# Optimization experiments

Hardware: AMD Instinct MI355X
Metric: run time of the kernel (lower is better)

The kernel has to match this reference:

```python
import jax, jax.numpy as jnp
import numpy as np

B, P, C, UP = 4, 512, 384, 4
K1, K2, KR = 16, 8, 16
NOISE_SCALE = 0.02


def setup_inputs() -> dict:
    key = jax.random.key(0)
    ks = jax.random.split(key, 32)
    w = lambda i, s: (jax.random.normal(ks[i], s, jnp.float32) * 0.02)
    return {
        "ctx_xyz": jax.random.normal(ks[0], (B, P, 3), jnp.float32),
        "ctx_tokens": jax.random.normal(ks[1], (B, P, C), jnp.float32),
        "pred_xyz": jax.random.normal(ks[2], (B, P, 3), jnp.float32),
        "pred_token": jax.random.normal(ks[3], (B, P, C), jnp.float32),
        "noise": jax.random.normal(ks[4], (B, P * UP, 3), jnp.float32),
        "conv1_w1": w(5, (2 * C, C // 2)), "conv1_b1": jnp.zeros((C // 2,), jnp.float32),
        "conv1_w2": w(6, (C // 2, C // 2)), "conv1_b2": jnp.zeros((C // 2,), jnp.float32),
        "conv2_w1": w(7, (2 * (C // 2), C // 4)), "conv2_b1": jnp.zeros((C // 4,), jnp.float32),
        "conv2_w2": w(8, (C // 4, C // 4)), "conv2_b2": jnp.zeros((C // 4,), jnp.float32),
        "cdef_w1": w(9, (C // 4, C // 4)), "cdef_b1": jnp.zeros((C // 4,), jnp.float32),
        "cdef_w2": w(10, (C // 4, 3)), "cdef_b2": jnp.zeros((3,), jnp.float32),
        "fold_w1": w(11, (C // 4 + 3, 256)), "fold_b1": jnp.zeros((256,), jnp.float32),
        "fold_w2": w(12, (256, 256)), "fold_b2": jnp.zeros((256,), jnp.float32),
        "fold_w3": w(13, (256, 3)), "fold_b3": jnp.zeros((3,), jnp.float32),
        "ref_w1": w(14, (2 * (C // 4 + 3), C)), "ref_b1": jnp.zeros((C,), jnp.float32),
        "ref_w2": w(15, (C, 3)), "ref_b2": jnp.zeros((3,), jnp.float32),
    }


def knn_idx(x, k):
    # x: [N, D]; k nearest neighbors by L2, no self-loops (as knn_graph loop=False)
    sq = jnp.sum(x * x, axis=1)
    d = sq[:, None] + sq[None, :] - 2.0 * (x @ x.T)  # [N, N]
    n = x.shape[0]
    d = d.at[jnp.arange(n), jnp.arange(n)].set(jnp.inf)
    return jax.lax.top_k(-d, k)[1]  # [N, k]


def edge_max(x, idx, mlp):
    # EdgeConv: out[i] = max_j mlp([x_i, x_j - x_i])
    n, k = idx.shape
    xi = jnp.broadcast_to(x[:, None, :], (n, k, x.shape[1]))
    xj = x[idx]  # [N, k, D]
    return jnp.max(mlp(jnp.concatenate([xi, xj - xi], axis=-1)), axis=1)


def mlp2(w1, b1, w2, b2):
    return lambda t: jnp.maximum(t @ w1 + b1, 0.0) @ w2 + b2


def reference(ctx_xyz, ctx_tokens, pred_xyz, pred_token, noise,
              conv1_w1, conv1_b1, conv1_w2, conv1_b2,
              conv2_w1, conv2_b1, conv2_w2, conv2_b2,
              cdef_w1, cdef_b1, cdef_w2, cdef_b2,
              fold_w1, fold_b1, fold_w2, fold_b2, fold_w3, fold_b3,
              ref_w1, ref_b1, ref_w2, ref_b2):
    def shared_edgeconv(x):
        h = edge_max(x, knn_idx(x, K1), mlp2(conv1_w1, conv1_b1, conv1_w2, conv1_b2))
        return edge_max(h, knn_idx(h, K2), mlp2(conv2_w1, conv2_b1, conv2_w2, conv2_b2))

    # context branch
    ctx_xyz_f = ctx_xyz.reshape(-1, 3)
    ctx_tok_f = ctx_tokens.reshape(-1, C)
    ctx_feat = shared_edgeconv(ctx_tok_f)                       # [B*P, C//4]
    ctx_xyz_out = ctx_xyz_f + 0.05 * mlp2(cdef_w1, cdef_b1, cdef_w2, cdef_b2)(ctx_feat)

    # target branch: upsample + assign tokens
    tgt_xyz = (jnp.repeat(pred_xyz, UP, axis=1) + NOISE_SCALE * noise).reshape(-1, 3)
    tgt_tok = jnp.repeat(ctx_tokens, UP, axis=1).reshape(-1, C)
    tgt_feat = shared_edgeconv(tgt_tok)                         # [B*P*UP, C//4]

    # folding MLP (Linear-ReLU-Linear-ReLU-Linear) residual
    h = jnp.concatenate([tgt_xyz, tgt_feat], axis=-1)
    h = jnp.maximum(h @ fold_w1 + fold_b1, 0.0)
    h = jnp.maximum(h @ fold_w2 + fold_b2, 0.0)
    tgt_xyz = tgt_xyz + h @ fold_w3 + fold_b3

    # GNN refiner: knn over xyz, EdgeConv over [feat, xyz]
    idx = knn_idx(tgt_xyz, KR)
    xcat = jnp.concatenate([tgt_feat, tgt_xyz], axis=-1)
    tgt_xyz = tgt_xyz + edge_max(xcat, idx, mlp2(ref_w1, ref_b1, ref_w2, ref_b2))

    return jnp.concatenate([ctx_xyz_out, tgt_xyz], axis=0)
```

## Files before the change

kernel.cpp:

```cpp
#include <hip/hip_runtime.h>

#define N2 2048
#define N8 8192
#define CDIM 384
#define H1C 192
#define H2C 96
#define PDIM 512
#define KRR 16
#define FOLDH 256
#define XCAP 256
#define XTILE 1024
#define INFF 3.0e38f

__device__ __forceinline__ float frelu(float x) { return x > 0.f ? x : 0.f; }

__device__ __forceinline__ void bitonic64_val(float& d, int lane) {
    #pragma unroll
    for (int k = 2; k <= 64; k <<= 1) {
        #pragma unroll
        for (int j = k >> 1; j > 0; j >>= 1) {
            float od = __shfl_xor(d, j);
            bool lower = (lane & j) == 0;
            bool olt = od < d;
            bool take = lower ? olt : !olt;
            if (lane & k) take = !take;
            if (take) d = od;
        }
    }
}

__device__ __forceinline__ void bitonic64_pair(float& d, int& c, int lane) {
    #pragma unroll
    for (int k = 2; k <= 64; k <<= 1) {
        #pragma unroll
        for (int j = k >> 1; j > 0; j >>= 1) {
            float od = __shfl_xor(d, j);
            int   oc = __shfl_xor(c, j);
            bool lower = (lane & j) == 0;
            bool olt = (od < d) || (od == d && oc < c);
            bool take = lower ? olt : !olt;
            if (lane & k) take = !take;
            if (take) { d = od; c = oc; }
        }
    }
}

__device__ __forceinline__ void select_slow(const float* bd, const int* bi, int cnt,
                                            int ksel, int row, int n, int* out, int lane) {
    float cd[4]; int cix[4];
    #pragma unroll
    for (int s = 0; s < 4; ++s) {
        int c = lane + 64*s;
        bool v = c < cnt;
        cd[s]  = v ? bd[c] : INFF;
        cix[s] = v ? bi[c] : 0x7fffffff;
    }
    for (int r = 0; r < ksel; ++r) {
        float lv = cd[0]; int li = cix[0];
        #pragma unroll
        for (int s = 1; s < 4; ++s) {
            if (cd[s] < lv || (cd[s] == lv && cix[s] < li)) { lv = cd[s]; li = cix[s]; }
        }
        float wv = lv; int wi = li;
        #pragma unroll
        for (int s = 1; s < 64; s <<= 1) {
            float ov = __shfl_xor(wv, s); int oi = __shfl_xor(wi, s);
            if (ov < wv || (ov == wv && oi < wi)) { wv = ov; wi = oi; }
        }
        if (lane == 0) {
            int safe = ((unsigned)wi < (unsigned)n) ? wi : ((row + 1) & (n - 1));
            out[row*ksel + r] = safe;
        }
        #pragma unroll
        for (int s = 0; s < 4; ++s) {
            if (cd[s] == wv && cix[s] == wi) { cd[s] = INFF; cix[s] = 0x7fffffff; }
        }
    }
}

__global__ __launch_bounds__(256) void rowsq_kernel(const float* __restrict__ x,
                                                    float* __restrict__ sq, int d) {
    int wave = threadIdx.x >> 6, lane = threadIdx.x & 63;
    int row = blockIdx.x*4 + wave;
    float acc = 0.f;
    for (int k = lane; k < d; k += 64) { float v = x[(size_t)row*d + k]; acc += v*v; }
    #pragma unroll
    for (int s = 1; s < 64; s <<= 1) acc += __shfl_xor(acc, s);
    if (lane == 0) sq[row] = acc;
}

__global__ __launch_bounds__(256) void rowsqpair_kernel(const float* __restrict__ xA,
                                                        float* __restrict__ sqA,
                                                        const float* __restrict__ xB,
                                                        float* __restrict__ sqB, int d) {
    const float* x = blockIdx.y ? xB : xA;
    float* sq = blockIdx.y ? sqB : sqA;
    int wave = threadIdx.x >> 6, lane = threadIdx.x & 63;
    int row = blockIdx.x*4 + wave;
    float acc = 0.f;
    for (int k = lane; k < d; k += 64) { float v = x[(size_t)row*d + k]; acc += v*v; }
    #pragma unroll
    for (int s = 1; s < 64; s <<= 1) acc += __shfl_xor(acc, s);
    if (lane == 0) sq[row] = acc;
}

__device__ __forceinline__ void disttri_body(const float* __restrict__ x, const float* __restrict__ sq,
                                             float* __restrict__ dist, int n, int K) {
    int l = blockIdx.x;
    int by = (int)((sqrtf(8.f*(float)l + 1.f) - 1.f)*0.5f);
    while ((by+1)*(by+2)/2 <= l) ++by;
    while (by*(by+1)/2 > l) --by;
    int bx = l - by*(by+1)/2;
    int row0 = by*64, col0 = bx*64;
    __shared__ __align__(16) float As[16][68];
    __shared__ __align__(16) float Bs[16][68];
    __shared__ __align__(16) float T[64][68];
    int tx = threadIdx.x, ty = threadIdx.y;
    int t = ty*16 + tx;
    float acc[4][4] = {};
    for (int k0 = 0; k0 < K; k0 += 16) {
        #pragma unroll
        for (int r = 0; r < 4; ++r) {
            int e = t + 256*r; int kk = e & 15, mm = e >> 4;
            As[kk][mm] = x[(size_t)(row0+mm)*K + k0+kk];
            Bs[kk][mm] = x[(size_t)(col0+mm)*K + k0+kk];
        }
        __syncthreads();
        #pragma unroll
        for (int kk = 0; kk < 16; ++kk) {
            float4 a4 = *(const float4*)&As[kk][ty*4];
            float4 b4 = *(const float4*)&Bs[kk][tx*4];
            acc[0][0] += a4.x*b4.x; acc[0][1] += a4.x*b4.y; acc[0][2] += a4.x*b4.z; acc[0][3] += a4.x*b4.w;
            acc[1][0] += a4.y*b4.x; acc[1][1] += a4.y*b4.y; acc[1][2] += a4.y*b4.z; acc[1][3] += a4.y*b4.w;
            acc[2][0] += a4.z*b4.x; acc[2][1] += a4.z*b4.y; acc[2][2] += a4.z*b4.z; acc[2][3] += a4.z*b4.w;
            acc[3][0] += a4.w*b4.x; acc[3][1] += a4.w*b4.y; acc[3][2] += a4.w*b4.z; acc[3][3] += a4.w*b4.w;
        }
        __syncthreads();
    }
    bool mirror = (row0 != col0);
    #pragma unroll
    for (int i2 = 0; i2 < 4; ++i2) {
        int row = row0 + ty*4 + i2;
        float sr = sq[row];
        float4 o;
        o.x = sr + sq[col0+tx*4+0] - 2.f*acc[i2][0];
        o.y = sr + sq[col0+tx*4+1] - 2.f*acc[i2][1];
        o.z = sr + sq[col0+tx*4+2] - 2.f*acc[i2][2];
        o.w = sr + sq[col0+tx*4+3] - 2.f*acc[i2][3];
        *(float4*)&dist[(size_t)row*n + col0 + tx*4] = o;
        if (mirror) {
            T[tx*4+0][ty*4+i2] = o.x;
            T[tx*4+1][ty*4+i2] = o.y;
            T[tx*4+2][ty*4+i2] = o.z;
            T[tx*4+3][ty*4+i2] = o.w;
        }
    }
    if (mirror) {
        __syncthreads();
        #pragma unroll
        for (int i2 = 0; i2 < 4; ++i2) {
            int orow = col0 + ty*4 + i2;
            float4 o = *(const float4*)&T[ty*4+i2][tx*4];
            *(float4*)&dist[(size_t)orow*n + row0 + tx*4] = o;
        }
    }
}

__global__ __launch_bounds__(256) void dist64tri_kernel(const float* __restrict__ x,
                                                        const float* __restrict__ sq,
                                                        float* __restrict__ dist, int n, int K) {
    disttri_body(x, sq, dist, n, K);
}

__global__ __launch_bounds__(256) void distpairtri_kernel(const float* __restrict__ xA,
                                                          const float* __restrict__ sqA,
                                                          float* __restrict__ dA,
                                                          const float* __restrict__ xB,
                                                          const float* __restrict__ sqB,
                                                          float* __restrict__ dB, int n, int K) {
    const float* x  = blockIdx.z ? xB : xA;
    const float* sq = blockIdx.z ? sqB : sqA;
    float* dist     = blockIdx.z ? dB : dA;
    disttri_body(x, sq, dist, n, K);
}

__device__ __forceinline__ void gemm_body(const float* __restrict__ A, const float* __restrict__ Bw,
                                          const float* __restrict__ BwB, const float* __restrict__ bias,
                                          float* __restrict__ C, int m, int K) {
    __shared__ __align__(16) float As[16][68];
    __shared__ __align__(16) float Bs[16][68];
    int tx = threadIdx.x, ty = threadIdx.y;
    int t = ty*16 + tx;
    int row0 = blockIdx.y*64, col0 = blockIdx.x*64;
    float acc[4][4] = {};
    for (int k0 = 0; k0 < K; k0 += 16) {
        #pragma unroll
        for (int r = 0; r < 4; ++r) {
            int e = t + 256*r; int kk = e & 15, mm = e >> 4;
            As[kk][mm] = (k0 + kk < K) ? A[(size_t)(row0+mm)*K + k0+kk] : 0.f;
        }
        #pragma unroll
        for (int r = 0; r < 4; ++r) {
            int e = t + 256*r; int nn = e & 63, kk = e >> 6;
            int col = col0 + nn, k = k0 + kk;
            float bv = 0.f;
            if (k < K && col < m) {
                bv = Bw[(size_t)k*m + col];
                if (BwB) bv -= BwB[(size_t)k*m + col];
            }
            Bs[kk][nn] = bv;
        }
        __syncthreads();
        #pragma unroll
        for (int kk = 0; kk < 16; ++kk) {
            float4 a4 = *(const float4*)&As[kk][ty*4];
            float4 b4 = *(const float4*)&Bs[kk][tx*4];
            acc[0][0] += a4.x*b4.x; acc[0][1] += a4.x*b4.y; acc[0][2] += a4.x*b4.z; acc[0][3] += a4.x*b4.w;
            acc[1][0] += a4.y*b4.x; acc[1][1] += a4.y*b4.y; acc[1][2] += a4.y*b4.z; acc[1][3] += a4.y*b4.w;
            acc[2][0] += a4.z*b4.x; acc[2][1] += a4.z*b4.y; acc[2][2] += a4.z*b4.z; acc[2][3] += a4.z*b4.w;
            acc[3][0] += a4.w*b4.x; acc[3][1] += a4.w*b4.y; acc[3][2] += a4.w*b4.z; acc[3][3] += a4.w*b4.w;
        }
        __syncthreads();
    }
    #pragma unroll
    for (int i2 = 0; i2 < 4; ++i2) {
        int row = row0 + ty*4 + i2;
        #pragma unroll
        for (int j2 = 0; j2 < 4; ++j2) {
            int col = col0 + tx*4 + j2;
            if (col < m) C[(size_t)row*m + col] = acc[i2][j2] + (bias ? bias[col] : 0.f);
        }
    }
}

__global__ __launch_bounds__(256) void gemmquad_kernel(
    const float* A0, const float* Bw0, const float* BwB0, const float* bias0, float* C0,
    const float* A1, const float* Bw1, const float* BwB1, const float* bias1, float* C1,
    const float* A2, const float* Bw2, const float* BwB2, const float* bias2, float* C2,
    const float* A3, const float* Bw3, const float* BwB3, const float* bias3, float* C3,
    int m, int K) {
    int z = blockIdx.z;
    const float* A    = (z==0)?A0 :(z==1)?A1 :(z==2)?A2 :A3;
    const float* Bw   = (z==0)?Bw0:(z==1)?Bw1:(z==2)?Bw2:Bw3;
    const float* BwB  = (z==0)?BwB0:(z==1)?BwB1:(z==2)?BwB2:BwB3;
    const float* bias = (z==0)?bias0:(z==1)?bias1:(z==2)?bias2:bias3;
    float* C          = (z==0)?C0 :(z==1)?C1 :(z==2)?C2 :C3;
    gemm_body(A, Bw, BwB, bias, C, m, K);
}

template<int EPT, int SELF, int EREAL, int IDXS, int YT>
__device__ __forceinline__ void edge_fused_body(const float* __restrict__ u, const float* __restrict__ v,
                                                const int* __restrict__ idx,
                                                const float* __restrict__ Bw, const float* __restrict__ bias,
                                                float* __restrict__ hout, int m, int K, int npts) {
    if ((int)blockIdx.y >= YT) return;
    constexpr int LOG2EPT = (EPT == 16) ? 4 : (EPT == 8) ? 3 : 2;
    __shared__ __align__(16) float As[16][68];
    __shared__ __align__(16) float Bs[16][68];
    int tx = threadIdx.x, ty = threadIdx.y;
    int t = ty*16 + tx;
    int row0 = blockIdx.y*64, col0 = blockIdx.x*64;
    float acc[4][4] = {};
    for (int k0 = 0; k0 < K; k0 += 16) {
        #pragma unroll
        for (int r = 0; r < 4; ++r) {
            int e_ = t + 256*r; int kk = e_ & 15, mm = e_ >> 4;
            int row = row0 + mm, k = k0 + kk;
            int i = row >> LOG2EPT;
            int e = row - (i << LOG2EPT);
            int j;
            if (SELF && e == 0) j = i;
            else if (e < EREAL) j = idx[i*IDXS + (e - SELF)];
            else j = i;
            j = ((unsigned)j < (unsigned)npts) ? j : i;
            As[kk][mm] = frelu(u[(size_t)i*K + k] + v[(size_t)j*K + k]);
        }
        #pragma unroll
        for (int r = 0; r < 4; ++r) {
            int e_ = t + 256*r; int nn = e_ & 63, kk = e_ >> 6;
            int col = col0 + nn;
            Bs[kk][nn] = (col < m) ? Bw[(size_t)(k0+kk)*m + col] : 0.f;
        }
        __syncthreads();
        #pragma unroll
        for (int kk = 0; kk < 16; ++kk) {
            float4 a4 = *(const float4*)&As[kk][ty*4];
            float4 b4 = *(const float4*)&Bs[kk][tx*4];
            acc[0][0] += a4.x*b4.x; acc[0][1] += a4.x*b4.y; acc[0][2] += a4.x*b4.z; acc[0][3] += a4.x*b4.w;
            acc[1][0] += a4.y*b4.x; acc[1][1] += a4.y*b4.y; acc[1][2] += a4.y*b4.z; acc[1][3] += a4.y*b4.w;
            acc[2][0] += a4.z*b4.x; acc[2][1] += a4.z*b4.y; acc[2][2] += a4.z*b4.z; acc[2][3] += a4.z*b4.w;
            acc[3][0] += a4.w*b4.x; acc[3][1] += a4.w*b4.y; acc[3][2] += a4.w*b4.z; acc[3][3] += a4.w*b4.w;
        }
        __syncthreads();
    }
    float bestv[4];
    #pragma unroll
    for (int j2 = 0; j2 < 4; ++j2)
        bestv[j2] = fmaxf(fmaxf(acc[0][j2], acc[1][j2]), fmaxf(acc[2][j2], acc[3][j2]));
    if (EPT >= 8) {
        #pragma unroll
        for (int j2 = 0; j2 < 4; ++j2) bestv[j2] = fmaxf(bestv[j2], __shfl_xor(bestv[j2], 16));
    }
    if (EPT == 16) {
        #pragma unroll
        for (int j2 = 0; j2 < 4; ++j2) bestv[j2] = fmaxf(bestv[j2], __shfl_xor(bestv[j2], 32));
    }
    bool writer; int p;
    if (EPT == 16) { writer = (ty & 3) == 0; p = (row0 >> 4) + (ty >> 2); }
    else if (EPT == 8) { writer = (ty & 1) == 0; p = (row0 >> 3) + (ty >> 1); }
    else { writer = true; p = (row0 >> 2) + ty; }
    if (writer) {
        #pragma unroll
        for (int j2 = 0; j2 < 4; ++j2) {
            int col = col0 + tx*4 + j2;
            if (col < m) hout[(size_t)p*m + col] = bestv[j2] + bias[col];
        }
    }
}

__global__ __launch_bounds__(256) void edge_fused1_kernel(const float* u1, const float* v1,
                                                          const int* cidx1,
                                                          const float* Bw, const float* bias,
                                                          float* h_ctx, float* h_tgt, int npts) {
    if (blockIdx.z == 0) edge_fused_body<16,0,16,16,512>(u1, v1, cidx1, Bw, bias, h_ctx, H1C, H1C, npts);
    else                 edge_fused_body<8,1,5,16,256>(u1, v1, cidx1, Bw, bias, h_tgt, H1C, H1C, npts);
}

__global__ __launch_bounds__(256) void edge_fused2_kernel(const float* u2c, const float* v2c,
                                                          const float* u2t, const float* v2t,
                                                          const int* cidx2, const int* tidx2,
                                                          const float* Bw, const float* bias,
                                                          float* cfeat, float* tfeat, int npts) {
    if (blockIdx.z == 0) edge_fused_body<8,0,8,8,256>(u2c, v2c, cidx2, Bw, bias, cfeat, H2C, H2C, npts);
    else                 edge_fused_body<4,1,3,2,128>(u2t, v2t, tidx2, Bw, bias, tfeat, H2C, H2C, npts);
}

__global__ __launch_bounds__(128) void cdef_kernel(const float* __restrict__ cfeat,
                                                   const float* __restrict__ cdw1, const float* __restrict__ cdb1,
                                                   const float* __restrict__ cdw2, const float* __restrict__ cdb2,
                                                   const float* __restrict__ ctx_xyz,
                                                   float* __restrict__ out_ctx) {
    int i = blockIdx.x, tid = threadIdx.x, wave = tid >> 6, lane = tid & 63;
    __shared__ float sf_[96], st2_[96];
    if (tid < 96) sf_[tid] = cfeat[(size_t)i*H2C + tid];
    __syncthreads();
    if (tid < 96) {
        float a = cdb1[tid];
        for (int k = 0; k < 96; ++k) a += sf_[k]*cdw1[k*96 + tid];
        st2_[tid] = frelu(a);
    }
    __syncthreads();
    if (wave == 0) {
        float s0 = st2_[lane];
        float p0 = s0*cdw2[lane*3+0], p1 = s0*cdw2[lane*3+1], p2 = s0*cdw2[lane*3+2];
        if (lane < 32) {
            float s1 = st2_[lane+64];
            p0 += s1*cdw2[(lane+64)*3+0];
            p1 += s1*cdw2[(lane+64)*3+1];
            p2 += s1*cdw2[(lane+64)*3+2];
        }
        #pragma unroll
        for (int s = 1; s < 64; s <<= 1) {
            p0 += __shfl_xor(p0, s); p1 += __shfl_xor(p1, s); p2 += __shfl_xor(p2, s);
        }
        if (lane == 0) {
            out_ctx[i*3+0] = ctx_xyz[i*3+0] + 0.05f*(cdb2[0] + p0);
            out_ctx[i*3+1] = ctx_xyz[i*3+1] + 0.05f*(cdb2[1] + p1);
            out_ctx[i*3+2] = ctx_xyz[i*3+2] + 0.05f*(cdb2[2] + p2);
        }
    }
}

__global__ __launch_bounds__(256) void gatherpair_kernel(
    const float* __restrict__ featd, const float* __restrict__ xyzg,
    const float* Bw0, const float* BwB0, const float* bias0, float* C0,
    const float* Bw1, const float* BwB1, const float* bias1, float* C1,
    int m, int K) {
    int z = blockIdx.z;
    const float* Bw   = z ? Bw1 : Bw0;
    const float* BwB  = z ? BwB1 : BwB0;
    const float* bias = z ? bias1 : bias0;
    float* C          = z ? C1 : C0;
    __shared__ __align__(16) float As[16][68];
    __shared__ __align__(16) float Bs[16][68];
    int tx = threadIdx.x, ty = threadIdx.y;
    int t = ty*16 + tx;
    int row0 = blockIdx.y*64, col0 = blockIdx.x*64;
    float acc[4][4] = {};
    for (int k0 = 0; k0 < K; k0 += 16) {
        #pragma unroll
        for (int r = 0; r < 4; ++r) {
            int e = t + 256*r; int kk = e & 15, mm = e >> 4;
            int k = k0 + kk, grow = row0 + mm;
            float av = 0.f;
            if (k < K) {
                if (k < 96) { int b = grow >> 11, p = (grow & 2047) >> 2;
                              av = featd[(size_t)(b*PDIM + p)*H2C + k]; }
                else av = xyzg[(size_t)grow*3 + (k - 96)];
            }
            As[kk][mm] = av;
        }
        #pragma unroll
        for (int r = 0; r < 4; ++r) {
            int e = t + 256*r; int nn = e & 63, kk = e >> 6;
            int col = col0 + nn, k = k0 + kk;
            float bv = 0.f;
            if (k < K && col < m) {
                bv = Bw[(size_t)k*m + col];
                if (BwB) bv -= BwB[(size_t)k*m + col];
            }
            Bs[kk][nn] = bv;
        }
        __syncthreads();
        #pragma unroll
        for (int kk = 0; kk < 16; ++kk) {
            float4 a4 = *(const float4*)&As[kk][ty*4];
            float4 b4 = *(const float4*)&Bs[kk][tx*4];
            acc[0][0] += a4.x*b4.x; acc[0][1] += a4.x*b4.y; acc[0][2] += a4.x*b4.z; acc[0][3] += a4.x*b4.w;
            acc[1][0] += a4.y*b4.x; acc[1][1] += a4.y*b4.y; acc[1][2] += a4.y*b4.z; acc[1][3] += a4.y*b4.w;
            acc[2][0] += a4.z*b4.x; acc[2][1] += a4.z*b4.y; acc[2][2] += a4.z*b4.z; acc[2][3] += a4.z*b4.w;
            acc[3][0] += a4.w*b4.x; acc[3][1] += a4.w*b4.y; acc[3][2] += a4.w*b4.z; acc[3][3] += a4.w*b4.w;
        }
        __syncthreads();
    }
    #pragma unroll
    for (int i2 = 0; i2 < 4; ++i2) {
        int row = row0 + ty*4 + i2;
        #pragma unroll
        for (int j2 = 0; j2 < 4; ++j2) {
            int col = col0 + tx*4 + j2;
            if (col < m) C[(size_t)row*m + col] = acc[i2][j2] + (bias ? bias[col] : 0.f);
        }
    }
}

__global__ __launch_bounds__(256) void knn_dist_rt_kernel(const float* __restrict__ dA,
                                                          const float* __restrict__ dB, int n,
                                                          int* __restrict__ outA, int* __restrict__ outB,
                                                          int kA, int kB, int nblkA) {
    int wave = threadIdx.x >> 6, lane = threadIdx.x & 63;
    bool useB = (int)blockIdx.x >= nblkA;
    const float* dist = useB ? dB : dA;
    int* out = useB ? outB : outA;
    int ksel = useB ? kB : kA;
    int bx = useB ? (int)blockIdx.x - nblkA : (int)blockIdx.x;
    int row = bx*4 + wave;
    __shared__ float bufd[4][XCAP];
    __shared__ int   bufi[4][XCAP];
    __shared__ int   lcnt[4];
    const float4* drow = (const float4*)(dist + (size_t)row*n);
    int nq = n >> 2;
    float mv = INFF;
    for (int i = lane; i < nq; i += 64) {
        float4 d4 = drow[i]; int base = i*4;
        float a = (base+0 == row) ? INFF : d4.x;
        float b = (base+1 == row) ? INFF : d4.y;
        float c = (base+2 == row) ? INFF : d4.z;
        float d = (base+3 == row) ? INFF : d4.w;
        mv = fminf(mv, fminf(fminf(a,b), fminf(c,d)));
    }
    float sd = mv;
    bitonic64_val(sd, lane);
    float Tv = __shfl(sd, ksel - 1);
    if (lane == 0) lcnt[wave] = 0;
    for (int i = lane; i < nq; i += 64) {
        float4 d4 = drow[i]; int base = i*4;
        float dv4[4] = {d4.x, d4.y, d4.z, d4.w};
        #pragma unroll
        for (int q = 0; q < 4; ++q) {
            int col = base + q;
            if (col != row && dv4[q] <= Tv) {
                int pos = atomicAdd(&lcnt[wave], 1);
                if (pos < XCAP) { bufd[wave][pos] = dv4[q]; bufi[wave][pos] = col; }
            }
        }
    }
    int cnt = lcnt[wave]; if (cnt > XCAP) cnt = XCAP;
    if (cnt <= 64) {
        float d = (lane < cnt) ? bufd[wave][lane] : INFF;
        int   c = (lane < cnt) ? bufi[wave][lane] : 0x7fffffff;
        bitonic64_pair(d, c, lane);
        if (lane < ksel) {
            int safe = ((unsigned)c < (unsigned)n) ? c : ((row + 1) & (n - 1));
            out[row*ksel + lane] = safe;
        }
    } else {
        select_slow(bufd[wave], bufi[wave], cnt, ksel, row, n, out, lane);
    }
}

__global__ __launch_bounds__(256) void knn_xyz16_kernel(const float4* __restrict__ pts, int n,
                                                        int* __restrict__ out_idx) {
    int tid = threadIdx.x, wave = tid >> 6, lane = tid & 63;
    int rbase = blockIdx.x*16 + wave*4;
    __shared__ __align__(16) float4 tile[XTILE];
    __shared__ float bufd[16][XCAP];
    __shared__ int   bufi[16][XCAP];
    __shared__ int   lcnt[16];
    float4 P0 = pts[rbase], P1 = pts[rbase+1], P2 = pts[rbase+2], P3 = pts[rbase+3];
    float mv0 = INFF, mv1 = INFF, mv2 = INFF, mv3 = INFF;
    for (int t0 = 0; t0 < n; t0 += XTILE) {
        __syncthreads();
        #pragma unroll
        for (int k = 0; k < XTILE/256; ++k) tile[tid + 256*k] = pts[t0 + tid + 256*k];
        __syncthreads();
        for (int c = lane; c < XTILE; c += 64) {
            float4 q = tile[c];
            int col = t0 + c;
            float d0 = P0.w + q.w - 2.f*(P0.x*q.x + P0.y*q.y + P0.z*q.z);
            float d1 = P1.w + q.w - 2.f*(P1.x*q.x + P1.y*q.y + P1.z*q.z);
            float d2 = P2.w + q.w - 2.f*(P2.x*q.x + P2.y*q.y + P2.z*q.z);
            float d3 = P3.w + q.w - 2.f*(P3.x*q.x + P3.y*q.y + P3.z*q.z);
            d0 = (col == rbase)   ? INFF : d0;
            d1 = (col == rbase+1) ? INFF : d1;
            d2 = (col == rbase+2) ? INFF : d2;
            d3 = (col == rbase+3) ? INFF : d3;
            mv0 = fminf(mv0, d0); mv1 = fminf(mv1, d1);
            mv2 = fminf(mv2, d2); mv3 = fminf(mv3, d3);
        }
    }
    bitonic64_val(mv0, lane); bitonic64_val(mv1, lane);
    bitonic64_val(mv2, lane); bitonic64_val(mv3, lane);
    float Tv0 = __shfl(mv0, 15), Tv1 = __shfl(mv1, 15);
    float Tv2 = __shfl(mv2, 15), Tv3 = __shfl(mv3, 15);
    if (lane < 4) lcnt[wave*4 + lane] = 0;
    for (int t0 = 0; t0 < n; t0 += XTILE) {
        __syncthreads();
        #pragma unroll
        for (int k = 0; k < XTILE/256; ++k) tile[tid + 256*k] = pts[t0 + tid + 256*k];
        __syncthreads();
        for (int c = lane; c < XTILE; c += 64) {
            float4 q = tile[c];
            int col = t0 + c;
            float d0 = P0.w + q.w - 2.f*(P0.x*q.x + P0.y*q.y + P0.z*q.z);
            float d1 = P1.w + q.w - 2.f*(P1.x*q.x + P1.y*q.y + P1.z*q.z);
            float d2 = P2.w + q.w - 2.f*(P2.x*q.x + P2.y*q.y + P2.z*q.z);
            float d3 = P3.w + q.w - 2.f*(P3.x*q.x + P3.y*q.y + P3.z*q.z);
            if (col != rbase && d0 <= Tv0) {
                int pos = atomicAdd(&lcnt[wave*4+0], 1);
                if (pos < XCAP) { bufd[wave*4+0][pos] = d0; bufi[wave*4+0][pos] = col; }
            }
            if (col != rbase+1 && d1 <= Tv1) {
                int pos = atomicAdd(&lcnt[wave*4+1], 1);
                if (pos < XCAP) { bufd[wave*4+1][pos] = d1; bufi[wave*4+1][pos] = col; }
            }
            if (col != rbase+2 && d2 <= Tv2) {
                int pos = atomicAdd(&lcnt[wave*4+2], 1);
                if (pos < XCAP) { bufd[wave*4+2][pos] = d2; bufi[wave*4+2][pos] = col; }
            }
            if (col != rbase+3 && d3 <= Tv3) {
                int pos = atomicAdd(&lcnt[wave*4+3], 1);
                if (pos < XCAP) { bufd[wave*4+3][pos] = d3; bufi[wave*4+3][pos] = col; }
            }
        }
    }
    for (int jj = 0; jj < 4; ++jj) {
        int brow = wave*4 + jj, row = rbase + jj;
        int cnt = lcnt[brow]; if (cnt > XCAP) cnt = XCAP;
        if (cnt <= 64) {
            float d = (lane < cnt) ? bufd[brow][lane] : INFF;
            int   c = (lane < cnt) ? bufi[brow][lane] : 0x7fffffff;
            bitonic64_pair(d, c, lane);
            if (lane < 16) {
                int safe = ((unsigned)c < (unsigned)n) ? c : ((row + 1) & (n - 1));
                out_idx[row*16 + lane] = safe;
            }
        } else {
            select_slow(bufd[brow], bufi[brow], cnt, 16, row, n, out_idx, lane);
        }
    }
}

__global__ __launch_bounds__(256) void edge_ref_kernel(const float* __restrict__ ur,
                                                       const float* __restrict__ vr,
                                                       const float* __restrict__ w2,
                                                       const float* __restrict__ b2,
                                                       const int* __restrict__ idx,
                                                       const float* __restrict__ xyz_in,
                                                       float* __restrict__ out, int n) {
    int wave = threadIdx.x >> 6, lane = threadIdx.x & 63;
    int i = blockIdx.x*4 + wave;
    if (i >= n) return;
    float m0 = -INFF, m1 = -INFF, m2 = -INFF;
    float uh[6];
    #pragma unroll
    for (int t = 0; t < 6; ++t) uh[t] = ur[(size_t)i*384 + lane + 64*t];
    for (int e = 0; e < KRR; ++e) {
        int j = idx[i*KRR + e];
        j = ((unsigned)j < (unsigned)n) ? j : i;
        float a0 = 0.f, a1 = 0.f, a2 = 0.f;
        #pragma unroll
        for (int t = 0; t < 6; ++t) {
            int h = lane + 64*t;
            float tv = frelu(uh[t] + vr[(size_t)j*384 + h]);
            a0 += tv*w2[h*3+0]; a1 += tv*w2[h*3+1]; a2 += tv*w2[h*3+2];
        }
        #pragma unroll
        for (int s = 32; s > 0; s >>= 1) {
            a0 += __shfl_xor(a0, s); a1 += __shfl_xor(a1, s); a2 += __shfl_xor(a2, s);
        }
        m0 = fmaxf(m0, a0 + b2[0]); m1 = fmaxf(m1, a1 + b2[1]); m2 = fmaxf(m2, a2 + b2[2]);
    }
    if (lane == 0) {
        out[i*3+0] = xyz_in[i*3+0] + m0;
        out[i*3+1] = xyz_in[i*3+1] + m1;
        out[i*3+2] = xyz_in[i*3+2] + m2;
    }
}

__global__ __launch_bounds__(256) void fold_kernel(const float* __restrict__ pred_xyz,
                                                   const float* __restrict__ noise,
                                                   const float* __restrict__ featd,
                                                   const float* __restrict__ w1, const float* __restrict__ b1,
                                                   const float* __restrict__ w2, const float* __restrict__ b2,
                                                   const float* __restrict__ w3, const float* __restrict__ b3,
                                                   float* __restrict__ xyz1, float4* __restrict__ pts_out) {
    const int PTS = 16;
    int base = blockIdx.x * PTS;
    int tid = threadIdx.x;
    __shared__ __align__(16) float xin[PTS][100];
    __shared__ __align__(16) float h1[PTS][FOLDH];
    __shared__ __align__(16) float h2s[PTS][FOLDH];
    __shared__ float oxyz[PTS][3];
    for (int t = tid; t < PTS*100; t += 256) {
        int pt = t/100, k = t - pt*100;
        int gi = base + pt;
        float vv = 0.f;
        if (k < 3) {
            int b = gi >> 11, p = (gi & 2047) >> 2;
            vv = pred_xyz[(size_t)(b*PDIM + p)*3 + k] + 0.02f*noise[(size_t)gi*3 + k];
        } else if (k < 99) {
            int b = gi >> 11, p = (gi & 2047) >> 2;
            vv = featd[(size_t)(b*PDIM + p)*H2C + (k - 3)];
        }
        xin[pt][k] = vv;
    }
    __syncthreads();
    int c = tid;
    float acc[PTS];
    #pragma unroll
    for (int pt = 0; pt < PTS; ++pt) acc[pt] = b1[c];
    for (int k0 = 0; k0 < 96; k0 += 4) {
        float wa = w1[(k0+0)*FOLDH + c], wb = w1[(k0+1)*FOLDH + c];
        float wc = w1[(k0+2)*FOLDH + c], wd = w1[(k0+3)*FOLDH + c];
        #pragma unroll
        for (int pt = 0; pt < PTS; ++pt) {
            float4 xv = *(const float4*)&xin[pt][k0];
            acc[pt] += xv.x*wa + xv.y*wb + xv.z*wc + xv.w*wd;
        }
    }
    {
        float wa = w1[96*FOLDH + c], wb = w1[97*FOLDH + c], wc = w1[98*FOLDH + c];
        #pragma unroll
        for (int pt = 0; pt < PTS; ++pt) {
            float4 xv = *(const float4*)&xin[pt][96];
            acc[pt] += xv.x*wa + xv.y*wb + xv.z*wc;
        }
    }
    #pragma unroll
    for (int pt = 0; pt < PTS; ++pt) h1[pt][c] = frelu(acc[pt]);
    __syncthreads();
    #pragma unroll
    for (int pt = 0; pt < PTS; ++pt) acc[pt] = b2[c];
    for (int k0 = 0; k0 < FOLDH; k0 += 4) {
        float wa = w2[(k0+0)*FOLDH + c], wb = w2[(k0+1)*FOLDH + c];
        float wc = w2[(k0+2)*FOLDH + c], wd = w2[(k0+3)*FOLDH + c];
        #pragma unroll
        for (int pt = 0; pt < PTS; ++pt) {
            float4 hv = *(const float4*)&h1[pt][k0];
            acc[pt] += hv.x*wa + hv.y*wb + hv.z*wc + hv.w*wd;
        }
    }
    #pragma unroll
    for (int pt = 0; pt < PTS; ++pt) h2s[pt][c] = frelu(acc[pt]);
    __syncthreads();
    if (tid < PTS*3) {
        int pt = tid/3, cc = tid - pt*3;
        float a = b3[cc];
        for (int k0 = 0; k0 < FOLDH; k0 += 4) {
            float4 hv = *(const float4*)&h2s[pt][k0];
            a += hv.x*w3[(k0+0)*3+cc] + hv.y*w3[(k0+1)*3+cc] + hv.z*w3[(k0+2)*3+cc] + hv.w*w3[(k0+3)*3+cc];
        }
        int gi = base + pt;
        float res = xin[pt][cc] + a;
        xyz1[(size_t)gi*3 + cc] = res;
        oxyz[pt][cc] = res;
    }
    __syncthreads();
    if (tid < PTS) {
        float x = oxyz[tid][0], y = oxyz[tid][1], z = oxyz[tid][2];
        pts_out[base + tid] = make_float4(x, y, z, x*x + y*y + z*z);
    }
}

extern "C" void kernel_launch(void* const* d_in, const int* in_sizes, int n_in,
                              void* d_out, int out_size, void* d_ws, size_t ws_size,
                              hipStream_t stream) {
    const float* ctx_xyz    = (const float*)d_in[0];
    const float* ctx_tokens = (const float*)d_in[1];
    const float* pred_xyz   = (const float*)d_in[2];
    const float* noise      = (const float*)d_in[4];
    const float* c1w1 = (const float*)d_in[5];
    const float* c1b1 = (const float*)d_in[6];
    const float* c1w2 = (const float*)d_in[7];
    const float* c1b2 = (const float*)d_in[8];
    const float* c2w1 = (const float*)d_in[9];
    const float* c2b1 = (const float*)d_in[10];
    const float* c2w2 = (const float*)d_in[11];
    const float* c2b2 = (const float*)d_in[12];
    const float* cdw1 = (const float*)d_in[13];
    const float* cdb1 = (const float*)d_in[14];
    const float* cdw2 = (const float*)d_in[15];
    const float* cdb2 = (const float*)d_in[16];
    const float* fw1  = (const float*)d_in[17];
    const float* fb1  = (const float*)d_in[18];
    const float* fw2  = (const float*)d_in[19];
    const float* fb2  = (const float*)d_in[20];
    const float* fw3  = (const float*)d_in[21];
    const float* fb3  = (const float*)d_in[22];
    const float* rw1  = (const float*)d_in[23];
    const float* rb1  = (const float*)d_in[24];
    const float* rw2  = (const float*)d_in[25];
    const float* rb2  = (const float*)d_in[26];

    float* W = (float*)d_ws;
    float* dist  = W;
    float* distB = W + 4194304;
    float* cfeat = W;
    float* ur    = W;
    float* vr    = W + 3145728;
    float* h_ctx = W + 8388608;
    float* h_tgt = h_ctx + 393216;
    float* UV    = h_tgt + 393216;
    float* u1  = UV;            float* v1  = UV + 393216;
    float* u2c = UV;            float* v2c = UV + 196608;
    float* u2t = UV + 393216;   float* v2t = UV + 589824;
    float* tfeat = UV + 786432;
    float* xyz1  = tfeat + 196608;
    float4* pts  = (float4*)(xyz1 + 24576);
    float* sqb     = (float*)pts + 32768;
    float* sq_hctx = sqb + N2;
    float* sq_htgt = sq_hctx + N2;
    int* cidx1 = (int*)(sq_htgt + N2);
    int* cidx2 = cidx1 + N2*16;
    int* tidx2 = cidx2 + N2*8;
    int* ridx  = tidx2 + N2*2;

    float* out_ctx = (float*)d_out;
    float* out_tgt = out_ctx + N2*3;

    dim3 b16(16, 16);
    const int NTRI = 32*33/2;
    const float* NUL = nullptr;

    rowsq_kernel<<<N2/4, 256, 0, stream>>>(ctx_tokens, sqb, CDIM);
    dist64tri_kernel<<<NTRI, b16, 0, stream>>>(ctx_tokens, sqb, dist, N2, CDIM);
    knn_dist_rt_kernel<<<N2/4, 256, 0, stream>>>(dist, dist, N2, cidx1, cidx1, 16, 16, N2/4);

    gemmquad_kernel<<<dim3(3, 32, 2), b16, 0, stream>>>(
        ctx_tokens, c1w1, c1w1 + 384*192, c1b1, u1,
        ctx_tokens, c1w1 + 384*192, NUL, NUL, v1,
        ctx_tokens, c1w1, NUL, NUL, u1,
        ctx_tokens, c1w1, NUL, NUL, v1,
        H1C, CDIM);
    edge_fused1_kernel<<<dim3(3, 512, 2), b16, 0, stream>>>(u1, v1, cidx1, c1w2, c1b2,
                                                            h_ctx, h_tgt, N2);
    rowsqpair_kernel<<<dim3(N2/4, 2), 256, 0, stream>>>(h_ctx, sq_hctx, h_tgt, sq_htgt, H1C);

    distpairtri_kernel<<<dim3(NTRI, 1, 2), b16, 0, stream>>>(h_ctx, sq_hctx, dist,
                                                             h_tgt, sq_htgt, distB, N2, H1C);
    knn_dist_rt_kernel<<<2*(N2/4), 256, 0, stream>>>(dist, distB, N2, cidx2, tidx2, 8, 2, N2/4);
    gemmquad_kernel<<<dim3(2, 32, 4), b16, 0, stream>>>(
        h_ctx, c2w1, c2w1 + 192*96, c2b1, u2c,
        h_ctx, c2w1 + 192*96, NUL, NUL, v2c,
        h_tgt, c2w1, c2w1 + 192*96, c2b1, u2t,
        h_tgt, c2w1 + 192*96, NUL, NUL, v2t,
        H2C, H1C);

    edge_fused2_kernel<<<dim3(2, 256, 2), b16, 0, stream>>>(u2c, v2c, u2t, v2t, cidx2, tidx2,
                                                            c2w2, c2b2, cfeat, tfeat, N2);
    cdef_kernel<<<N2, 128, 0, stream>>>(cfeat, cdw1, cdb1, cdw2, cdb2, ctx_xyz, out_ctx);

    fold_kernel<<<N8/16, 256, 0, stream>>>(pred_xyz, noise, tfeat, fw1, fb1, fw2, fb2, fw3, fb3, xyz1, pts);

    knn_xyz16_kernel<<<N8/16, 256, 0, stream>>>(pts, N8, ridx);

    gatherpair_kernel<<<dim3(6, N8/64, 2), b16, 0, stream>>>(
        tfeat, xyz1,
        rw1, rw1 + 99*384, rb1, ur,
        rw1 + 99*384, NUL, NUL, vr,
        384, 99);
    edge_ref_kernel<<<N8/4, 256, 0, stream>>>(ur, vr, rw2, rb2, ridx, xyz1, out_tgt, N8);
}
```

Before: 465.8 us.

## Vectorize edge GEMM tile loads and shrink knn candidate buffer with inline selection

The fused edge GEMM now computes each thread's gathered row and neighbor index once, then loads u/v and weight tiles as float4 instead of scalar gathers that repeat the index lookup. The xyz kNN kernel halves its per-row candidate buffer capacity, which cuts shared memory per block, and replaces the generic slow select with a wave-wide iterative argmin over two register slots. The smaller cap can drop candidates when more than 128 pass the threshold, which could change the neighbors chosen. The float4 loads also assume K and m are multiples of 4 and that the pointers are 16-byte aligned.

```diff
diff --git a/kernel.cpp b/kernel.cpp
--- a/kernel.cpp
+++ b/kernel.cpp
@@ -9,6 +9,7 @@
 #define KRR 16
 #define FOLDH 256
 #define XCAP 256
+#define XCAPX 128
 #define XTILE 1024
 #define INFF 3.0e38f
 
@@ -260,26 +261,36 @@
     int tx = threadIdx.x, ty = threadIdx.y;
     int t = ty*16 + tx;
     int row0 = blockIdx.y*64, col0 = blockIdx.x*64;
+    int mmA = t >> 2;
+    int kqA = (t & 3) * 4;
+    int rowA = row0 + mmA;
+    int iA = rowA >> LOG2EPT;
+    int eA = rowA - (iA << LOG2EPT);
+    int jA;
+    if (SELF && eA == 0) jA = iA;
+    else if (eA < EREAL) jA = idx[iA*IDXS + (eA - SELF)];
+    else jA = iA;
+    jA = ((unsigned)jA < (unsigned)npts) ? jA : iA;
+    const float* uRow = u + (size_t)iA*K + kqA;
+    const float* vRow = v + (size_t)jA*K + kqA;
+    int nnB = (t & 15) * 4, kkB = t >> 4;
     float acc[4][4] = {};
     for (int k0 = 0; k0 < K; k0 += 16) {
-        #pragma unroll
-        for (int r = 0; r < 4; ++r) {
-            int e_ = t + 256*r; int kk = e_ & 15, mm = e_ >> 4;
-            int row = row0 + mm, k = k0 + kk;
-            int i = row >> LOG2EPT;
-            int e = row - (i << LOG2EPT);
-            int j;
-            if (SELF && e == 0) j = i;
-            else if (e < EREAL) j = idx[i*IDXS + (e - SELF)];
-            else j = i;
-            j = ((unsigned)j < (unsigned)npts) ? j : i;
-            As[kk][mm] = frelu(u[(size_t)i*K + k] + v[(size_t)j*K + k]);
-        }
-        #pragma unroll
-        for (int r = 0; r < 4; ++r) {
-            int e_ = t + 256*r; int nn = e_ & 63, kk = e_ >> 6;
-            int col = col0 + nn;
-            Bs[kk][nn] = (col < m) ? Bw[(size_t)(k0+kk)*m + col] : 0.f;
+        float4 u4 = *(const float4*)(uRow + k0);
+        float4 v4 = *(const float4*)(vRow + k0);
+        As[kqA+0][mmA] = frelu(u4.x + v4.x);
+        As[kqA+1][mmA] = frelu(u4.y + v4.y);
+        As[kqA+2][mmA] = frelu(u4.z + v4.z);
+        As[kqA+3][mmA] = frelu(u4.w + v4.w);
+        int colB = col0 + nnB;
+        if (colB + 3 < m) {
+            *(float4*)&Bs[kkB][nnB] = *(const float4*)&Bw[(size_t)(k0+kkB)*m + colB];
+        } else {
+            #pragma unroll
+            for (int q = 0; q < 4; ++q) {
+                int col = colB + q;
+                Bs[kkB][nnB+q] = (col < m) ? Bw[(size_t)(k0+kkB)*m + col] : 0.f;
+            }
         }
         __syncthreads();
         #pragma unroll
@@ -494,8 +505,8 @@
     int tid = threadIdx.x, wave = tid >> 6, lane = tid & 63;
     int rbase = blockIdx.x*16 + wave*4;
     __shared__ __align__(16) float4 tile[XTILE];
-    __shared__ float bufd[16][XCAP];
-    __shared__ int   bufi[16][XCAP];
+    __shared__ float bufd[16][XCAPX];
+    __shared__ int   bufi[16][XCAPX];
     __shared__ int   lcnt[16];
     float4 P0 = pts[rbase], P1 = pts[rbase+1], P2 = pts[rbase+2], P3 = pts[rbase+3];
     float mv0 = INFF, mv1 = INFF, mv2 = INFF, mv3 = INFF;
@@ -538,25 +549,25 @@
             float d3 = P3.w + q.w - 2.f*(P3.x*q.x + P3.y*q.y + P3.z*q.z);
             if (col != rbase && d0 <= Tv0) {
                 int pos = atomicAdd(&lcnt[wave*4+0], 1);
-                if (pos < XCAP) { bufd[wave*4+0][pos] = d0; bufi[wave*4+0][pos] = col; }
+                if (pos < XCAPX) { bufd[wave*4+0][pos] = d0; bufi[wave*4+0][pos] = col; }
             }
             if (col != rbase+1 && d1 <= Tv1) {
                 int pos = atomicAdd(&lcnt[wave*4+1], 1);
-                if (pos < XCAP) { bufd[wave*4+1][pos] = d1; bufi[wave*4+1][pos] = col; }
+                if (pos < XCAPX) { bufd[wave*4+1][pos] = d1; bufi[wave*4+1][pos] = col; }
             }
             if (col != rbase+2 && d2 <= Tv2) {
                 int pos = atomicAdd(&lcnt[wave*4+2], 1);
-                if (pos < XCAP) { bufd[wave*4+2][pos] = d2; bufi[wave*4+2][pos] = col; }
+                if (pos < XCAPX) { bufd[wave*4+2][pos] = d2; bufi[wave*4+2][pos] = col; }
             }
             if (col != rbase+3 && d3 <= Tv3) {
                 int pos = atomicAdd(&lcnt[wave*4+3], 1);
-                if (pos < XCAP) { bufd[wave*4+3][pos] = d3; bufi[wave*4+3][pos] = col; }
+                if (pos < XCAPX) { bufd[wave*4+3][pos] = d3; bufi[wave*4+3][pos] = col; }
             }
         }
     }
     for (int jj = 0; jj < 4; ++jj) {
         int brow = wave*4 + jj, row = rbase + jj;
-        int cnt = lcnt[brow]; if (cnt > XCAP) cnt = XCAP;
+        int cnt = lcnt[brow]; if (cnt > XCAPX) cnt = XCAPX;
         if (cnt <= 64) {
             float d = (lane < cnt) ? bufd[brow][lane] : INFF;
             int   c = (lane < cnt) ? bufi[brow][lane] : 0x7fffffff;
@@ -566,7 +577,32 @@
                 out_idx[row*16 + lane] = safe;
             }
         } else {
-            select_slow(bufd[brow], bufi[brow], cnt, 16, row, n, out_idx, lane);
+            float cd[2]; int cix[2];
+            #pragma unroll
+            for (int s = 0; s < 2; ++s) {
+                int c = lane + 64*s;
+                bool v = c < cnt;
+                cd[s]  = v ? bufd[brow][c] : INFF;
+                cix[s] = v ? bufi[brow][c] : 0x7fffffff;
+            }
+            for (int r = 0; r < 16; ++r) {
+                float lv = cd[0]; int li = cix[0];
+                if (cd[1] < lv || (cd[1] == lv && cix[1] < li)) { lv = cd[1]; li = cix[1]; }
+                float wv = lv; int wi = li;
+                #pragma unroll
+                for (int s = 1; s < 64; s <<= 1) {
+                    float ov = __shfl_xor(wv, s); int oi = __shfl_xor(wi, s);
+                    if (ov < wv || (ov == wv && oi < wi)) { wv = ov; wi = oi; }
+                }
+                if (lane == 0) {
+                    int safe = ((unsigned)wi < (unsigned)n) ? wi : ((row + 1) & (n - 1));
+                    out_idx[row*16 + r] = safe;
+                }
+                #pragma unroll
+                for (int s = 0; s < 2; ++s) {
+                    if (cd[s] == wv && cix[s] == wi) { cd[s] = INFF; cix[s] = 0x7fffffff; }
+                }
+            }
         }
     }
 }
```

New measurement: 447.6 us. -3.9%, faster.
